# Optimization experiments

Hardware: AMD Instinct MI355X
Metric: run time of the kernel (lower is better)

The kernel has to match this reference:

```python
import jax, jax.numpy as jnp
import numpy as np

# Faithful JAX translation of fastmax_function with mask=True, p=1, normalize=0.
# In that branch the torch code sets temperature = 1 and uses a0 = a1 = 1.

def setup_inputs() -> dict:
    key = jax.random.key(0)
    kq, kk, kv = jax.random.split(key, 3)
    b, h, n, d = 2, 8, 8192, 32
    q = jax.random.normal(kq, (b, h, n, d), dtype=jnp.float32)
    k = jax.random.normal(kk, (b, h, n, d), dtype=jnp.float32)
    v = jax.random.normal(kv, (b, h, n, d), dtype=jnp.float32)
    return {"q": q, "k": k, "v": v}


def reference(q, k, v):
    # q, k, v: (b, h, n, d); causal (mask=True), p=1, a0=a1=1, temperature=1
    b, h, n, d = q.shape
    # first term: running sum of values
    first = jnp.cumsum(v, axis=2)                                  # (b,h,n,d)
    # second term: q_i . (sum_{j<=i} k_j v_j^T)
    kv = jnp.einsum('bhnd,bhne->bhnde', k, v)                      # (b,h,n,d,d)
    kv_cs = jnp.cumsum(kv, axis=2)                                 # (b,h,n,d,d)
    second = jnp.einsum('bhnd,bhnde->bhne', q, kv_cs)              # (b,h,n,d)
    # denominator: i + q_i . (sum_{j<=i} k_j)
    k_cs = jnp.cumsum(k, axis=2)                                   # (b,h,n,d)
    div1 = jnp.arange(1, n + 1, dtype=q.dtype)                     # (n,)
    div2 = jnp.einsum('bhnd,bhnd->bhn', q, k_cs)                   # (b,h,n)
    div = (div1[None, None, :] + div2)[..., None]                  # (b,h,n,1)
    return (first + second) / div
```

## Files before the change

### kernel.cpp

```cpp
#include <hip/hip_runtime.h>


#define D      32
#define C      64
#define NCHUNK 128
#define BH     16
#define NSEQ   8192
#define STATE  1088

typedef __attribute__((ext_vector_type(8))) short bf16x8;
typedef __attribute__((ext_vector_type(4))) float f32x4;
typedef __attribute__((ext_vector_type(4))) unsigned short u16x4;

__device__ __forceinline__ unsigned short f2bf(float x) {
  union { float f; unsigned u; } c; c.f = x;
  unsigned r = (c.u + 0x7FFFu + ((c.u >> 16) & 1u)) >> 16;
  return (unsigned short)r;
}

__device__ __forceinline__ int permcol(int e) {
  return (e & 1) ? (16 + (e >> 1)) : (e >> 1);
}

__global__ __launch_bounds__(256) void chunk_state_kernel(
    const float* __restrict__ k, const float* __restrict__ v,
    float* __restrict__ states) {
  int blk = blockIdx.x;
  const float4* kp = (const float4*)k + (size_t)blk * 512;
  const float4* vp = (const float4*)v + (size_t)blk * 512;

  __shared__ __align__(16) unsigned short kT[D * 72];
  __shared__ __align__(16) unsigned short vT[D * 72];
  __shared__ __align__(16) float4 psK[256];
  __shared__ __align__(16) float4 psV[256];

  int t  = threadIdx.x;
  int j0 = t >> 3;
  int cb = (t & 7) * 4;
  float4 kA = kp[t], kB = kp[t + 256];
  float4 vA = vp[t], vB = vp[t + 256];

  const float* ka = &kA.x; const float* kb = &kB.x;
  const float* va = &vA.x; const float* vb = &vB.x;
#pragma unroll
  for (int cc = 0; cc < 4; ++cc) {
    kT[(cb + cc) * 72 + j0]      = f2bf(ka[cc]);
    kT[(cb + cc) * 72 + j0 + 32] = f2bf(kb[cc]);
    vT[(cb + cc) * 72 + j0]      = f2bf(va[cc]);
    vT[(cb + cc) * 72 + j0 + 32] = f2bf(vb[cc]);
  }
  psK[t] = make_float4(kA.x + kB.x, kA.y + kB.y, kA.z + kB.z, kA.w + kB.w);
  psV[t] = make_float4(vA.x + vB.x, vA.y + vB.y, vA.z + vB.z, vA.w + vB.w);
  __syncthreads();

  int lane = t & 63, w = t >> 6;
  int m16 = lane & 15, quad = lane >> 4;
  int mb = w >> 1, nb = w & 1;
  f32x4 acc = {0.f, 0.f, 0.f, 0.f};
#pragma unroll
  for (int kb2 = 0; kb2 < 2; ++kb2) {
    bf16x8 a = *(const bf16x8*)&kT[(16 * mb + m16) * 72 + kb2 * 32 + quad * 8];
    bf16x8 b = *(const bf16x8*)&vT[(16 * nb + m16) * 72 + kb2 * 32 + quad * 8];
    acc = __builtin_amdgcn_mfma_f32_16x16x32_bf16(a, b, acc, 0, 0, 0);
  }
  float* st = states + (size_t)blk * STATE;
#pragma unroll
  for (int reg = 0; reg < 4; ++reg) {
    int d1 = 16 * mb + quad * 4 + reg;
    int d2 = 16 * nb + m16;
    st[d1 * 32 + d2] = acc[reg];
  }
  if (t < 64) {
    int ee = t & 31;
    const float* ps = (t < 32) ? (const float*)psK : (const float*)psV;
    float s = 0.f;
#pragma unroll
    for (int m = 0; m < 32; ++m) s += ps[ee + 32 * m];
    st[1024 + ((t < 32) ? ee : 32 + ee)] = s;
  }
}

__global__ __launch_bounds__(256) void scan_kernel(float* __restrict__ states) {
  int gidx = blockIdx.x * 256 + threadIdx.x;
  int bh = gidx / STATE;
  int e  = gidx % STATE;
  float* base = states + (size_t)bh * NCHUNK * STATE + e;
  float a = 0.f;
#pragma unroll 1
  for (int c0 = 0; c0 < NCHUNK; c0 += 32) {
    float s[32];
#pragma unroll
    for (int r = 0; r < 32; ++r) s[r] = base[(size_t)(c0 + r) * STATE];
#pragma unroll
    for (int r = 0; r < 32; ++r) { float tv = s[r]; s[r] = a; a += tv; }
#pragma unroll
    for (int r = 0; r < 32; ++r) base[(size_t)(c0 + r) * STATE] = s[r];
  }
}

__global__ __launch_bounds__(256) void output_kernel(
    const float* __restrict__ q, const float* __restrict__ k,
    const float* __restrict__ v, const float* __restrict__ states,
    float* __restrict__ out) {
  int blk = blockIdx.x;
  int c   = blk & 127;
  size_t off = (size_t)blk * (C * D);
  const float4* qp4 = (const float4*)q + (size_t)blk * 512;
  const float4* kp4 = (const float4*)k + (size_t)blk * 512;
  const float4* vp4 = (const float4*)v + (size_t)blk * 512;
  const float4* st4 = (const float4*)(states + (size_t)blk * STATE);

  __shared__ __align__(16) unsigned short qbf[C * 40];
  __shared__ __align__(16) unsigned short kbf[C * 40];
  __shared__ __align__(16) unsigned short vTbf[D * 72];
  __shared__ __align__(16) unsigned short kvTbf[D * 40];
  __shared__ __align__(16) unsigned short Tbf[C * 72];
  __shared__ __align__(16) float q_s[C * 36];
  __shared__ __align__(16) float kc_s[C * 36];
  __shared__ __align__(16) float gtot[8 * 32];
  __shared__ __align__(16) float kpre_s[D], vpre_s[D], invdiv_s[C];

  int t  = threadIdx.x;
  int j0 = t >> 3;
  int cb = (t & 7) * 4;

  float4 qA = qp4[t], qB = qp4[t + 256];
  float4 kA = kp4[t], kB = kp4[t + 256];
  float4 vA = vp4[t], vB = vp4[t + 256];
  float4 sv = st4[t];
  float4 tail = make_float4(0.f, 0.f, 0.f, 0.f);
  if (t < 16) tail = st4[256 + t];

  for (int z = t; z < (C * 72) / 8; z += 256)
    ((uint4*)Tbf)[z] = make_uint4(0, 0, 0, 0);

  *(float4*)&q_s[j0 * 36 + cb]        = qA;
  *(float4*)&q_s[(j0 + 32) * 36 + cb] = qB;
  *(float4*)&kc_s[j0 * 36 + cb]        = kA;
  *(float4*)&kc_s[(j0 + 32) * 36 + cb] = kB;
  *(u16x4*)&qbf[j0 * 40 + cb] =
      (u16x4){f2bf(qA.x), f2bf(qA.y), f2bf(qA.z), f2bf(qA.w)};
  *(u16x4*)&qbf[(j0 + 32) * 40 + cb] =
      (u16x4){f2bf(qB.x), f2bf(qB.y), f2bf(qB.z), f2bf(qB.w)};
  *(u16x4*)&kbf[j0 * 40 + cb] =
      (u16x4){f2bf(kA.x), f2bf(kA.y), f2bf(kA.z), f2bf(kA.w)};
  *(u16x4*)&kbf[(j0 + 32) * 40 + cb] =
      (u16x4){f2bf(kB.x), f2bf(kB.y), f2bf(kB.z), f2bf(kB.w)};
  {
    const float* va = &vA.x; const float* vb = &vB.x;
    const float* sp = &sv.x;
#pragma unroll
    for (int cc = 0; cc < 4; ++cc) {
      int n = permcol(cb + cc);
      vTbf[n * 72 + j0]      = f2bf(va[cc]);
      vTbf[n * 72 + j0 + 32] = f2bf(vb[cc]);
      kvTbf[n * 40 + j0]     = f2bf(sp[cc]);
    }
  }
  if (t < 8)            ((float4*)kpre_s)[t]     = tail;
  else if (t < 16)      ((float4*)vpre_s)[t - 8] = tail;
  __syncthreads();

  int lane = t & 63, w = t >> 6;
  int m16 = lane & 15, quad = lane >> 4;

  const bf16x8 aQ = *(const bf16x8*)&qbf[(16 * w + m16) * 40 + quad * 8];
  for (int jb = 0; jb <= w; ++jb) {
    bf16x8 bK = *(const bf16x8*)&kbf[(16 * jb + m16) * 40 + quad * 8];
    f32x4 cS = {0.f, 0.f, 0.f, 0.f};
    cS = __builtin_amdgcn_mfma_f32_16x16x32_bf16(aQ, bK, cS, 0, 0, 0);
    int jcol = 16 * jb + m16;
#pragma unroll
    for (int reg = 0; reg < 4; ++reg) {
      int i = 16 * w + quad * 4 + reg;
      float tv = (jcol <= i) ? (1.f + cS[reg]) : 0.f;
      Tbf[i * 72 + jcol] = f2bf(tv);
    }
  }
  int rg = t >> 5;
  int e  = t & 31;
  float vals[8];
  {
    float run = 0.f;
#pragma unroll
    for (int r = 0; r < 8; ++r) {
      vals[r] = kc_s[(rg * 8 + r) * 36 + e];
      run += vals[r];
    }
    gtot[rg * 32 + e] = run;
  }
  __syncthreads();

  {
    float offv = kpre_s[e];
    for (int g = 0; g < rg; ++g) offv += gtot[g * 32 + e];
    float cacc = offv;
#pragma unroll
    for (int r = 0; r < 8; ++r) {
      cacc += vals[r];
      kc_s[(rg * 8 + r) * 36 + e] = cacc;
    }
  }
  __syncthreads();

  if (t < 64) {
    int i = t;
    float dp = 0.f;
#pragma unroll
    for (int d4 = 0; d4 < 8; ++d4) {
      float4 qv = *(const float4*)&q_s[i * 36 + 4 * d4];
      float4 kc = *(const float4*)&kc_s[i * 36 + 4 * d4];
      dp += qv.x * kc.x + qv.y * kc.y + qv.z * kc.z + qv.w * kc.w;
    }
    invdiv_s[i] = 1.f / ((float)(c * C + i + 1) + dp);
  }
  f32x4 o0 = {0.f, 0.f, 0.f, 0.f}, o1 = {0.f, 0.f, 0.f, 0.f};
  {
    bf16x8 b0 = *(const bf16x8*)&kvTbf[(m16)      * 40 + quad * 8];
    bf16x8 b1 = *(const bf16x8*)&kvTbf[(16 + m16) * 40 + quad * 8];
    o0 = __builtin_amdgcn_mfma_f32_16x16x32_bf16(aQ, b0, o0, 0, 0, 0);
    o1 = __builtin_amdgcn_mfma_f32_16x16x32_bf16(aQ, b1, o1, 0, 0, 0);
  }
  int kbcnt = (w >= 2) ? 2 : 1;
  for (int kb = 0; kb < kbcnt; ++kb) {
    bf16x8 aT = *(const bf16x8*)&Tbf[(16 * w + m16) * 72 + kb * 32 + quad * 8];
    bf16x8 b0 = *(const bf16x8*)&vTbf[(m16)      * 72 + kb * 32 + quad * 8];
    bf16x8 b1 = *(const bf16x8*)&vTbf[(16 + m16) * 72 + kb * 32 + quad * 8];
    o0 = __builtin_amdgcn_mfma_f32_16x16x32_bf16(aT, b0, o0, 0, 0, 0);
    o1 = __builtin_amdgcn_mfma_f32_16x16x32_bf16(aT, b1, o1, 0, 0, 0);
  }
  __syncthreads();

  int e0 = 2 * m16;
#pragma unroll
  for (int reg = 0; reg < 4; ++reg) {
    int i = 16 * w + quad * 4 + reg;
    float id = invdiv_s[i];
    float2 o;
    o.x = (vpre_s[e0]     + o0[reg]) * id;
    o.y = (vpre_s[e0 + 1] + o1[reg]) * id;
    *(float2*)&out[off + (size_t)i * D + e0] = o;
  }
}

extern "C" void kernel_launch(void* const* d_in, const int* in_sizes, int n_in,
                              void* d_out, int out_size, void* d_ws, size_t ws_size,
                              hipStream_t stream) {
  const float* q = (const float*)d_in[0];
  const float* k = (const float*)d_in[1];
  const float* v = (const float*)d_in[2];
  float* out    = (float*)d_out;
  float* states = (float*)d_ws;

  chunk_state_kernel<<<BH * NCHUNK, 256, 0, stream>>>(k, v, states);
  scan_kernel<<<(BH * STATE) / 256, 256, 0, stream>>>(states);
  output_kernel<<<BH * NCHUNK, 256, 0, stream>>>(q, k, v, states, out);
}
```

Before: 108.9 us.

## Fuse chunk-state computation and scan into grouped kernel with per-group totals

Drops the separate scan kernel. Each block now handles 8 consecutive chunks and keeps a running prefix of the chunk states in registers. It writes exclusive within-group prefixes plus a per-group total, and the output kernel adds the totals of earlier groups when it loads its state. This removes one launch and the strided scan over the states array, but the state kernel now runs only 256 blocks, each looping serially over 8 chunks. The output kernel also does up to 15 extra state reads per block.

```diff
diff --git a/kernel.cpp b/kernel.cpp
--- a/kernel.cpp
+++ b/kernel.cpp
@@ -4,8 +4,10 @@
 #define D      32
 #define C      64
 #define NCHUNK 128
+#define GSIZE  8
+#define NGROUP 16
 #define BH     16
-#define NSEQ   8192
+#define NBLK   (BH * NCHUNK)
 #define STATE  1088
 
 typedef __attribute__((ext_vector_type(8))) short bf16x8;
@@ -22,12 +24,17 @@
   return (e & 1) ? (16 + (e >> 1)) : (e >> 1);
 }
 
-__global__ __launch_bounds__(256) void chunk_state_kernel(
+__device__ __forceinline__ float4 add4(float4 a, float4 b) {
+  return make_float4(a.x + b.x, a.y + b.y, a.z + b.z, a.w + b.w);
+}
+
+__global__ __launch_bounds__(256) void state_scan_kernel(
     const float* __restrict__ k, const float* __restrict__ v,
-    float* __restrict__ states) {
+    float* __restrict__ states, float* __restrict__ totals) {
   int blk = blockIdx.x;
-  const float4* kp = (const float4*)k + (size_t)blk * 512;
-  const float4* vp = (const float4*)v + (size_t)blk * 512;
+  int c0  = blk * GSIZE;
+  const float4* kp = (const float4*)k + (size_t)c0 * 512;
+  const float4* vp = (const float4*)v + (size_t)c0 * 512;
 
   __shared__ __align__(16) unsigned short kT[D * 72];
   __shared__ __align__(16) unsigned short vT[D * 72];
@@ -37,78 +44,89 @@
   int t  = threadIdx.x;
   int j0 = t >> 3;
   int cb = (t & 7) * 4;
-  float4 kA = kp[t], kB = kp[t + 256];
-  float4 vA = vp[t], vB = vp[t + 256];
-
-  const float* ka = &kA.x; const float* kb = &kB.x;
-  const float* va = &vA.x; const float* vb = &vB.x;
-#pragma unroll
-  for (int cc = 0; cc < 4; ++cc) {
-    kT[(cb + cc) * 72 + j0]      = f2bf(ka[cc]);
-    kT[(cb + cc) * 72 + j0 + 32] = f2bf(kb[cc]);
-    vT[(cb + cc) * 72 + j0]      = f2bf(va[cc]);
-    vT[(cb + cc) * 72 + j0 + 32] = f2bf(vb[cc]);
-  }
-  psK[t] = make_float4(kA.x + kB.x, kA.y + kB.y, kA.z + kB.z, kA.w + kB.w);
-  psV[t] = make_float4(vA.x + vB.x, vA.y + vB.y, vA.z + vB.z, vA.w + vB.w);
-  __syncthreads();
-
   int lane = t & 63, w = t >> 6;
   int m16 = lane & 15, quad = lane >> 4;
   int mb = w >> 1, nb = w & 1;
-  f32x4 acc = {0.f, 0.f, 0.f, 0.f};
-#pragma unroll
-  for (int kb2 = 0; kb2 < 2; ++kb2) {
-    bf16x8 a = *(const bf16x8*)&kT[(16 * mb + m16) * 72 + kb2 * 32 + quad * 8];
-    bf16x8 b = *(const bf16x8*)&vT[(16 * nb + m16) * 72 + kb2 * 32 + quad * 8];
-    acc = __builtin_amdgcn_mfma_f32_16x16x32_bf16(a, b, acc, 0, 0, 0);
-  }
-  float* st = states + (size_t)blk * STATE;
-#pragma unroll
-  for (int reg = 0; reg < 4; ++reg) {
-    int d1 = 16 * mb + quad * 4 + reg;
-    int d2 = 16 * nb + m16;
-    st[d1 * 32 + d2] = acc[reg];
-  }
-  if (t < 64) {
-    int ee = t & 31;
-    const float* ps = (t < 32) ? (const float*)psK : (const float*)psV;
-    float s = 0.f;
-#pragma unroll
-    for (int m = 0; m < 32; ++m) s += ps[ee + 32 * m];
-    st[1024 + ((t < 32) ? ee : 32 + ee)] = s;
-  }
-}
-
-__global__ __launch_bounds__(256) void scan_kernel(float* __restrict__ states) {
-  int gidx = blockIdx.x * 256 + threadIdx.x;
-  int bh = gidx / STATE;
-  int e  = gidx % STATE;
-  float* base = states + (size_t)bh * NCHUNK * STATE + e;
-  float a = 0.f;
-#pragma unroll 1
-  for (int c0 = 0; c0 < NCHUNK; c0 += 32) {
-    float s[32];
-#pragma unroll
-    for (int r = 0; r < 32; ++r) s[r] = base[(size_t)(c0 + r) * STATE];
-#pragma unroll
-    for (int r = 0; r < 32; ++r) { float tv = s[r]; s[r] = a; a += tv; }
-#pragma unroll
-    for (int r = 0; r < 32; ++r) base[(size_t)(c0 + r) * STATE] = s[r];
-  }
+  int d1b = 16 * mb + quad * 4;
+  int d2  = 16 * nb + m16;
+
+  float pref[4] = {0.f, 0.f, 0.f, 0.f};
+  float tailpref = 0.f;
+
+  float4 kA = kp[t], kB = kp[t + 256];
+  float4 vA = vp[t], vB = vp[t + 256];
+
+  for (int ci = 0; ci < GSIZE; ++ci) {
+    {
+      const float* ka = &kA.x; const float* kb = &kB.x;
+      const float* va = &vA.x; const float* vb = &vB.x;
+#pragma unroll
+      for (int cc = 0; cc < 4; ++cc) {
+        kT[(cb + cc) * 72 + j0]      = f2bf(ka[cc]);
+        kT[(cb + cc) * 72 + j0 + 32] = f2bf(kb[cc]);
+        vT[(cb + cc) * 72 + j0]      = f2bf(va[cc]);
+        vT[(cb + cc) * 72 + j0 + 32] = f2bf(vb[cc]);
+      }
+      psK[t] = make_float4(kA.x + kB.x, kA.y + kB.y, kA.z + kB.z, kA.w + kB.w);
+      psV[t] = make_float4(vA.x + vB.x, vA.y + vB.y, vA.z + vB.z, vA.w + vB.w);
+    }
+    __syncthreads();
+
+    if (ci + 1 < GSIZE) {
+      const float4* kn = kp + (size_t)(ci + 1) * 512;
+      const float4* vn = vp + (size_t)(ci + 1) * 512;
+      kA = kn[t]; kB = kn[t + 256];
+      vA = vn[t]; vB = vn[t + 256];
+    }
+
+    f32x4 acc = {0.f, 0.f, 0.f, 0.f};
+#pragma unroll
+    for (int kb2 = 0; kb2 < 2; ++kb2) {
+      bf16x8 a = *(const bf16x8*)&kT[(16 * mb + m16) * 72 + kb2 * 32 + quad * 8];
+      bf16x8 b = *(const bf16x8*)&vT[(16 * nb + m16) * 72 + kb2 * 32 + quad * 8];
+      acc = __builtin_amdgcn_mfma_f32_16x16x32_bf16(a, b, acc, 0, 0, 0);
+    }
+    float csum = 0.f;
+    if (t < 64) {
+      int ee = t & 31;
+      const float* ps = (t < 32) ? (const float*)psK : (const float*)psV;
+#pragma unroll
+      for (int m = 0; m < 32; ++m) csum += ps[ee + 32 * m];
+    }
+
+    float* stC = states + (size_t)(c0 + ci) * STATE;
+#pragma unroll
+    for (int reg = 0; reg < 4; ++reg) {
+      stC[(d1b + reg) * 32 + d2] = pref[reg];
+      pref[reg] += acc[reg];
+    }
+    if (t < 64) {
+      stC[1024 + t] = tailpref;
+      tailpref += csum;
+    }
+    __syncthreads();
+  }
+
+  float* tp = totals + (size_t)blk * STATE;
+#pragma unroll
+  for (int reg = 0; reg < 4; ++reg) tp[(d1b + reg) * 32 + d2] = pref[reg];
+  if (t < 64) tp[1024 + t] = tailpref;
 }
 
 __global__ __launch_bounds__(256) void output_kernel(
     const float* __restrict__ q, const float* __restrict__ k,
     const float* __restrict__ v, const float* __restrict__ states,
-    float* __restrict__ out) {
+    const float* __restrict__ totals, float* __restrict__ out) {
   int blk = blockIdx.x;
   int c   = blk & 127;
+  int bh  = blk >> 7;
+  int g   = c >> 3;
   size_t off = (size_t)blk * (C * D);
   const float4* qp4 = (const float4*)q + (size_t)blk * 512;
   const float4* kp4 = (const float4*)k + (size_t)blk * 512;
   const float4* vp4 = (const float4*)v + (size_t)blk * 512;
   const float4* st4 = (const float4*)(states + (size_t)blk * STATE);
+  const float4* tb4 = (const float4*)(totals + (size_t)(bh * NGROUP) * STATE);
 
   __shared__ __align__(16) unsigned short qbf[C * 40];
   __shared__ __align__(16) unsigned short kbf[C * 40];
@@ -131,11 +149,27 @@
   float4 tail = make_float4(0.f, 0.f, 0.f, 0.f);
   if (t < 16) tail = st4[256 + t];
 
+  {
+    float4 a0 = make_float4(0.f, 0.f, 0.f, 0.f), a1 = a0, a2 = a0, a3 = a0;
+    int gp = 0;
+    for (; gp + 4 <= g; gp += 4) {
+      a0 = add4(a0, tb4[(size_t)(gp + 0) * 272 + t]);
+      a1 = add4(a1, tb4[(size_t)(gp + 1) * 272 + t]);
+      a2 = add4(a2, tb4[(size_t)(gp + 2) * 272 + t]);
+      a3 = add4(a3, tb4[(size_t)(gp + 3) * 272 + t]);
+    }
+    for (; gp < g; ++gp) a0 = add4(a0, tb4[(size_t)gp * 272 + t]);
+    sv = add4(sv, add4(add4(a0, a1), add4(a2, a3)));
+    if (t < 16)
+      for (int g2 = 0; g2 < g; ++g2)
+        tail = add4(tail, tb4[(size_t)g2 * 272 + 256 + t]);
+  }
+
   for (int z = t; z < (C * 72) / 8; z += 256)
     ((uint4*)Tbf)[z] = make_uint4(0, 0, 0, 0);
 
-  *(float4*)&q_s[j0 * 36 + cb]        = qA;
-  *(float4*)&q_s[(j0 + 32) * 36 + cb] = qB;
+  *(float4*)&q_s[j0 * 36 + cb]         = qA;
+  *(float4*)&q_s[(j0 + 32) * 36 + cb]  = qB;
   *(float4*)&kc_s[j0 * 36 + cb]        = kA;
   *(float4*)&kc_s[(j0 + 32) * 36 + cb] = kB;
   *(u16x4*)&qbf[j0 * 40 + cb] =
@@ -193,7 +227,7 @@
 
   {
     float offv = kpre_s[e];
-    for (int g = 0; g < rg; ++g) offv += gtot[g * 32 + e];
+    for (int g2 = 0; g2 < rg; ++g2) offv += gtot[g2 * 32 + e];
     float cacc = offv;
 #pragma unroll
     for (int r = 0; r < 8; ++r) {
@@ -222,10 +256,10 @@
     o1 = __builtin_amdgcn_mfma_f32_16x16x32_bf16(aQ, b1, o1, 0, 0, 0);
   }
   int kbcnt = (w >= 2) ? 2 : 1;
-  for (int kb = 0; kb < kbcnt; ++kb) {
-    bf16x8 aT = *(const bf16x8*)&Tbf[(16 * w + m16) * 72 + kb * 32 + quad * 8];
-    bf16x8 b0 = *(const bf16x8*)&vTbf[(m16)      * 72 + kb * 32 + quad * 8];
-    bf16x8 b1 = *(const bf16x8*)&vTbf[(16 + m16) * 72 + kb * 32 + quad * 8];
+  for (int kb2 = 0; kb2 < kbcnt; ++kb2) {
+    bf16x8 aT = *(const bf16x8*)&Tbf[(16 * w + m16) * 72 + kb2 * 32 + quad * 8];
+    bf16x8 b0 = *(const bf16x8*)&vTbf[(m16)      * 72 + kb2 * 32 + quad * 8];
+    bf16x8 b1 = *(const bf16x8*)&vTbf[(16 + m16) * 72 + kb2 * 32 + quad * 8];
     o0 = __builtin_amdgcn_mfma_f32_16x16x32_bf16(aT, b0, o0, 0, 0, 0);
     o1 = __builtin_amdgcn_mfma_f32_16x16x32_bf16(aT, b1, o1, 0, 0, 0);
   }
@@ -251,8 +285,8 @@
   const float* v = (const float*)d_in[2];
   float* out    = (float*)d_out;
   float* states = (float*)d_ws;
-
-  chunk_state_kernel<<<BH * NCHUNK, 256, 0, stream>>>(k, v, states);
-  scan_kernel<<<(BH * STATE) / 256, 256, 0, stream>>>(states);
-  output_kernel<<<BH * NCHUNK, 256, 0, stream>>>(q, k, v, states, out);
-}
+  float* totals = states + (size_t)NBLK * STATE;
+
+  state_scan_kernel<<<BH * NGROUP, 256, 0, stream>>>(k, v, states, totals);
+  output_kernel<<<NBLK, 256, 0, stream>>>(q, k, v, states, totals, out);
+}
```

Result: slower. 111.0 us (+2.0%).
